# Performance work log

Hardware: AMD Instinct MI355X
Metric: run time of the kernel (lower is better)

## Reference

```python
import jax, jax.numpy as jnp
import numpy as np

M, TS, NX, NY = 24, 60, 192, 192   # solutions, source timesteps, source grid
H, D = 4, 8                         # num_heads, d_head
SIGMA = 0.2
N_TIME_STEPS = 50
T_MAX = 200.0
LX = 100.0                          # solutions[0]['params']['Lx']
SRC_T_MAX = 200.0                   # solutions[0]['params']['t_max']
NG = 50                             # target grid resolution (hard-coded in source)


def setup_inputs():
    key = jax.random.key(0)
    ks = jax.random.split(key, 8)
    c1_preds = jax.random.normal(ks[0], (M, TS, NX, NY), jnp.float32)
    c2_preds = jax.random.normal(ks[1], (M, TS, NX, NY), jnp.float32)
    lys = 30.0 + 90.0 * jax.random.uniform(ks[2], (M,), jnp.float32)
    c_cus = 0.0029 * jax.random.uniform(ks[3], (M,), jnp.float32)
    c_nis = 0.0018 * jax.random.uniform(ks[4], (M,), jnp.float32)
    params = jnp.stack([lys, c_cus, c_nis], axis=1)  # [M,3]
    # nonuniform, sorted per-solution y grid spanning [0, Ly_m]
    base = jnp.linspace(0.0, 1.0, NY, dtype=jnp.float32) ** 1.2
    src_y = lys[:, None] * base[None, :]  # [M,NY]
    src_t_last = 100.0 + 200.0 * jax.random.uniform(ks[5], (M,), jnp.float32)
    Wq = 0.3 * jax.random.normal(ks[6], (3, H * D), jnp.float32)
    Wk = 0.3 * jax.random.normal(ks[7], (3, H * D), jnp.float32)
    bq = jnp.zeros((H * D,), jnp.float32)
    bk = jnp.zeros((H * D,), jnp.float32)
    return dict(c1_preds=c1_preds, c2_preds=c2_preds, params=params, src_y=src_y,
                src_t_last=src_t_last, Wq=Wq, bq=bq, Wk=Wk, bk=bk,
                ly_target=jnp.float32(75.0), c_cu_target=jnp.float32(0.0015),
                c_ni_target=jnp.float32(0.0009))


def _axis_interp(grid, q):
    """1-D linear interp setup. grid [G] sorted, q [P] -> (idx, frac, in_bounds)."""
    G = grid.shape[-1]
    idx = jnp.clip(jnp.searchsorted(grid, q, side='right') - 1, 0, G - 2)
    g0 = jnp.take(grid, idx)
    g1 = jnp.take(grid, idx + 1)
    frac = (q - g0) / (g1 - g0)
    inb = (q >= grid[0]) & (q <= grid[-1])  # scipy fill_value=0 outside
    return idx, frac, inb


def reference(c1_preds, c2_preds, params, src_y, src_t_last, Wq, bq, Wk, bk,
              ly_target, c_cu_target, c_ni_target):
    lys, c_cus, c_nis = params[:, 0], params[:, 1], params[:, 2]
    # normalization exactly as in the torch forward
    ly_n = (lys - 30.0) / (120.0 - 30.0)
    cu_n = c_cus / 0.0029
    ni_n = c_nis / 0.0018
    t_ly = (ly_target - 30.0) / (120.0 - 30.0)
    t_cu = c_cu_target / 0.0029
    t_ni = c_ni_target / 0.0018

    p = jnp.stack([ly_n, cu_n, ni_n], axis=1)            # [M,3]
    tgt = jnp.stack([t_ly, t_cu, t_ni])[None, :]          # [1,3]
    Q = (tgt @ Wq + bq).reshape(H, D)                     # [H,D]
    K = (p @ Wk + bk).reshape(-1, H, D)                   # [M,H,D]
    logits = jnp.einsum('mhd,hd->mh', K, Q) / jnp.sqrt(jnp.float32(D))
    attn = jax.nn.softmax(logits, axis=0).mean(axis=1)    # softmax over solutions, mean heads -> [M]

    dist2 = ((ly_n - t_ly) ** 2 + (cu_n - t_cu) ** 2 + (ni_n - t_ni) ** 2) / SIGMA ** 2
    sw = jnp.exp(-dist2 / 2.0)
    sw = sw / (sw.sum() + 1e-12)
    w = attn * sw
    w = w / (w.sum() + 1e-12)
    w = jax.lax.stop_gradient(w)  # original detaches weights before interpolation

    # ---- physics-aware interpolation ----
    times = jnp.linspace(0.0, min(SRC_T_MAX, T_MAX), N_TIME_STEPS)  # [T]
    ti = jnp.clip(jnp.round(times[:, None] / src_t_last[None, :] * (TS - 1)).astype(jnp.int32),
                  0, TS - 1)                                         # [T,M]

    src_x = jnp.linspace(0.0, LX, NX)
    qx = jnp.linspace(0.0, LX, NG)
    qy = (jnp.arange(NG, dtype=jnp.float32) / (NG - 1)) * ly_target  # linspace(0, ly_target, NG)

    ix, fx, mx = _axis_interp(src_x, qx)                             # [NG] each (shared x grid)
    scale = ly_target / lys                                           # [M]
    y_scaled = src_y * scale[:, None]                                 # [M,NY]
    iy, fy, my = jax.vmap(lambda g: _axis_interp(g, qy))(y_scaled)    # [M,NG] each
    mask = (mx[None, :, None] & my[:, None, :]).astype(c1_preds.dtype)  # [M,NG,NG]

    T = N_TIME_STEPS
    iy_b = jnp.broadcast_to(iy[None, :, None, :], (T, M, NG, NG))
    iy1_b = jnp.broadcast_to((iy + 1)[None, :, None, :], (T, M, NG, NG))

    def interp_field(preds):
        vals = preds[jnp.arange(M)[None, :], ti]                      # [T,M,NX,NY] time gather
        fxc = fx[None, None, :, None]
        vx = vals[:, :, ix, :] * (1.0 - fxc) + vals[:, :, ix + 1, :] * fxc  # [T,M,NG,NY]
        v0 = jnp.take_along_axis(vx, iy_b, axis=3)                    # [T,M,NG,NG]
        v1 = jnp.take_along_axis(vx, iy1_b, axis=3)
        fyc = fy[None, :, None, :]
        v = (v0 * (1.0 - fyc) + v1 * fyc) * mask[None]
        return jnp.einsum('tmij,m->tij', v, w)                        # weighted sum over solutions

    c1 = interp_field(c1_preds).at[:, :, 0].set(c_cu_target)
    c2 = interp_field(c2_preds).at[:, :, -1].set(c_ni_target)
    return jnp.stack([c1, c2])  # [2, T, NG, NG]
```

## Files before the change

kernel.cpp:

```cpp
#include <hip/hip_runtime.h>
#include <math.h>

#define M   24
#define TS  60
#define NX  192
#define NY  192
#define H_  4
#define D_  8
#define NTS 50
#define NG  50

__device__ float g_w[M];
__device__ int   g_ti[NTS][M];
__device__ int   g_ix[NG];
__device__ float g_fx[NG];
__device__ float g_mx[NG];
__device__ int   g_iy[M][NG];
__device__ float g_fy[M][NG];
__device__ float g_my[M][NG];

__global__ __launch_bounds__(256) void prep_init_kernel(
    const float* __restrict__ params, const float* __restrict__ src_y,
    const float* __restrict__ stl,
    const float* __restrict__ Wq, const float* __restrict__ bq,
    const float* __restrict__ Wk, const float* __restrict__ bk,
    const float* __restrict__ lyt_p, const float* __restrict__ ccu_p,
    const float* __restrict__ cni_p,
    float* __restrict__ out)
{
    const int tid = threadIdx.x;

    if (blockIdx.x > 0) {
        const int idx = (blockIdx.x - 1) * blockDim.x + tid;
        const int total = 2 * NTS * NG * NG;
        if (idx < total) {
            const int j = idx % NG;
            const int f = idx / (NTS * NG * NG);
            float v = 0.0f;
            if (f == 0 && j == 0)    v = ccu_p[0];
            if (f == 1 && j == NG-1) v = cni_p[0];
            out[idx] = v;
        }
        return;
    }

    __shared__ float s_logits[M][H_];
    __shared__ float s_sw[M];

    const float ly_target = lyt_p[0];
    const float c_cu_t = ccu_p[0];
    const float c_ni_t = cni_p[0];

    const float t_ly = (ly_target - 30.0f) / 90.0f;
    const float t_cu = c_cu_t / 0.0029f;
    const float t_ni = c_ni_t / 0.0018f;

    if (tid < M) {
        const int m = tid;
        const float ly  = params[m*3 + 0];
        const float ccu = params[m*3 + 1];
        const float cni = params[m*3 + 2];
        const float ly_n = (ly - 30.0f) / 90.0f;
        const float cu_n = ccu / 0.0029f;
        const float ni_n = cni / 0.0018f;
        for (int h = 0; h < H_; ++h) {
            float acc = 0.0f;
            for (int d = 0; d < D_; ++d) {
                const int col = h*D_ + d;
                const float q = t_ly*Wq[0*32+col] + t_cu*Wq[1*32+col] + t_ni*Wq[2*32+col] + bq[col];
                const float k = ly_n*Wk[0*32+col] + cu_n*Wk[1*32+col] + ni_n*Wk[2*32+col] + bk[col];
                acc += k * q;
            }
            s_logits[m][h] = acc / sqrtf(8.0f);
        }
        const float dly = ly_n - t_ly, dcu = cu_n - t_cu, dni = ni_n - t_ni;
        const float d2 = (dly*dly + dcu*dcu + dni*dni) / 0.04f;
        s_sw[m] = expf(-d2 * 0.5f);
    }
    __syncthreads();

    if (tid == 0) {
        float attn[M];
        for (int m = 0; m < M; ++m) attn[m] = 0.0f;
        for (int h = 0; h < H_; ++h) {
            float mxv = -1e30f;
            for (int m = 0; m < M; ++m) mxv = fmaxf(mxv, s_logits[m][h]);
            float e[M]; float s = 0.0f;
            for (int m = 0; m < M; ++m) { e[m] = expf(s_logits[m][h] - mxv); s += e[m]; }
            for (int m = 0; m < M; ++m) attn[m] += e[m] / s;
        }
        float ssw = 0.0f;
        for (int m = 0; m < M; ++m) ssw += s_sw[m];
        float w[M]; float wsum = 0.0f;
        for (int m = 0; m < M; ++m) {
            w[m] = (attn[m] * 0.25f) * (s_sw[m] / (ssw + 1e-12f));
            wsum += w[m];
        }
        for (int m = 0; m < M; ++m) g_w[m] = w[m] / (wsum + 1e-12f);
    }

    const float step_t = 200.0f / 49.0f;
    for (int idx = tid; idx < NTS*M; idx += blockDim.x) {
        const int t = idx / M, m = idx % M;
        const float tt = (t == NTS-1) ? 200.0f : step_t * (float)t;
        const float r = tt / stl[m] * 59.0f;
        int ti = (int)rintf(r);
        ti = ti < 0 ? 0 : (ti > TS-1 ? TS-1 : ti);
        g_ti[t][m] = ti;
    }

    if (tid < NG) {
        const int i = tid;
        const float step_x = 100.0f / 191.0f;
        const float step_q = 100.0f / 49.0f;
        const float q = (i == NG-1) ? 100.0f : step_q * (float)i;
        int pos = 0;
        for (int g = 0; g < NX; ++g) {
            const float gv = (g == NX-1) ? 100.0f : step_x * (float)g;
            if (gv <= q) pos = g + 1;
        }
        int id = pos - 1;
        id = id < 0 ? 0 : (id > NX-2 ? NX-2 : id);
        const float g0 = (id   == NX-1) ? 100.0f : step_x * (float)id;
        const float g1 = (id+1 == NX-1) ? 100.0f : step_x * (float)(id+1);
        g_ix[i] = id;
        g_fx[i] = (q - g0) / (g1 - g0);
        g_mx[i] = (q >= 0.0f && q <= 100.0f) ? 1.0f : 0.0f;
    }

    for (int idx = tid; idx < M*NG; idx += blockDim.x) {
        const int m = idx / NG, j = idx % NG;
        const float scale = ly_target / params[m*3 + 0];
        const float q = (float)j / 49.0f * ly_target;
        const float* sy = src_y + m*NY;
        int pos = 0;
        for (int g = 0; g < NY; ++g) {
            const float gv = sy[g] * scale;
            if (gv <= q) pos = g + 1;
        }
        int id = pos - 1;
        id = id < 0 ? 0 : (id > NY-2 ? NY-2 : id);
        const float g0 = sy[id] * scale;
        const float g1 = sy[id+1] * scale;
        g_iy[m][j] = id;
        g_fy[m][j] = (q - g0) / (g1 - g0);
        const float gfirst = sy[0] * scale;
        const float glast  = sy[NY-1] * scale;
        g_my[m][j] = (q >= gfirst && q <= glast) ? 1.0f : 0.0f;
    }
}

__global__ __launch_bounds__(256) void interp_kernel(
    const float* __restrict__ c1, const float* __restrict__ c2,
    float* __restrict__ out)
{
    const int m = blockIdx.x;
    const int t = blockIdx.y;
    const int f = blockIdx.z;
    const int tid = threadIdx.x;

    __shared__ float xrow[NG][NY + 1];

    const float* __restrict__ preds = (f == 0) ? c1 : c2;
    const int tim = g_ti[t][m];
    const float* __restrict__ slice = preds + (((size_t)m * TS + tim) * NX) * (size_t)NY;

    for (int idx = tid; idx < NG * (NY / 4); idx += blockDim.x) {
        const int i  = idx / (NY / 4);
        const int y4 = (idx - i * (NY / 4)) * 4;
        const int   ixi = g_ix[i];
        const float fxi = g_fx[i];
        const float4 r0 = *(const float4*)(slice + (size_t)ixi * NY + y4);
        const float4 r1 = *(const float4*)(slice + (size_t)(ixi + 1) * NY + y4);
        xrow[i][y4 + 0] = r0.x * (1.0f - fxi) + r1.x * fxi;
        xrow[i][y4 + 1] = r0.y * (1.0f - fxi) + r1.y * fxi;
        xrow[i][y4 + 2] = r0.z * (1.0f - fxi) + r1.z * fxi;
        xrow[i][y4 + 3] = r0.w * (1.0f - fxi) + r1.w * fxi;
    }
    __syncthreads();

    const float wm = g_w[m];
    for (int idx = tid; idx < NG * NG; idx += blockDim.x) {
        const int i = idx / NG;
        const int j = idx - i * NG;
        if ((f == 0 && j == 0) || (f == 1 && j == NG - 1)) continue;
        const int   iyj = g_iy[m][j];
        const float fyj = g_fy[m][j];
        const float msk = g_mx[i] * g_my[m][j];
        const float v0 = xrow[i][iyj];
        const float v1 = xrow[i][iyj + 1];
        const float v = (v0 * (1.0f - fyj) + v1 * fyj) * msk;
        atomicAdd(&out[(((size_t)f * NTS + t) * NG + i) * NG + j], v * wm);
    }
}

extern "C" void kernel_launch(void* const* d_in, const int* in_sizes, int n_in,
                              void* d_out, int out_size, void* d_ws, size_t ws_size,
                              hipStream_t stream) {
    const float* c1     = (const float*)d_in[0];
    const float* c2     = (const float*)d_in[1];
    const float* params = (const float*)d_in[2];
    const float* src_y  = (const float*)d_in[3];
    const float* stl    = (const float*)d_in[4];
    const float* Wq     = (const float*)d_in[5];
    const float* bq     = (const float*)d_in[6];
    const float* Wk     = (const float*)d_in[7];
    const float* bk     = (const float*)d_in[8];
    const float* lyt    = (const float*)d_in[9];
    const float* ccut   = (const float*)d_in[10];
    const float* cnit   = (const float*)d_in[11];
    float* out = (float*)d_out;

    const int total = 2 * NTS * NG * NG;
    const int init_blocks = (total + 255) / 256;
    prep_init_kernel<<<1 + init_blocks, 256, 0, stream>>>(
        params, src_y, stl, Wq, bq, Wk, bk, lyt, ccut, cnit, out);

    dim3 grid(M, NTS, 2);
    interp_kernel<<<grid, 256, 0, stream>>>(c1, c2, out);
}
```

Before: 436.8 us.

## Replace atomic accumulation with per-solution partial buffers and a reduce kernel

Instead of each (m,t,f) block atomically adding weighted values into the output, each block now writes its weighted slab to a workspace partial buffer, and a separate reduce kernel sums over the 24 solutions and applies the boundary overrides. The zero-init pass is dropped from the prep kernel. The shared-memory row is padded to allow float4 stores. This removes atomic contention, at the cost of writing and re-reading a 24x larger intermediate (about 29 MB) and an extra launch.

```diff
diff --git a/kernel.cpp b/kernel.cpp
--- a/kernel.cpp
+++ b/kernel.cpp
@@ -19,31 +19,15 @@
 __device__ float g_fy[M][NG];
 __device__ float g_my[M][NG];
 
-__global__ __launch_bounds__(256) void prep_init_kernel(
+__global__ __launch_bounds__(256) void prep_kernel(
     const float* __restrict__ params, const float* __restrict__ src_y,
     const float* __restrict__ stl,
     const float* __restrict__ Wq, const float* __restrict__ bq,
     const float* __restrict__ Wk, const float* __restrict__ bk,
     const float* __restrict__ lyt_p, const float* __restrict__ ccu_p,
-    const float* __restrict__ cni_p,
-    float* __restrict__ out)
+    const float* __restrict__ cni_p)
 {
     const int tid = threadIdx.x;
-
-    if (blockIdx.x > 0) {
-        const int idx = (blockIdx.x - 1) * blockDim.x + tid;
-        const int total = 2 * NTS * NG * NG;
-        if (idx < total) {
-            const int j = idx % NG;
-            const int f = idx / (NTS * NG * NG);
-            float v = 0.0f;
-            if (f == 0 && j == 0)    v = ccu_p[0];
-            if (f == 1 && j == NG-1) v = cni_p[0];
-            out[idx] = v;
-        }
-        return;
-    }
-
     __shared__ float s_logits[M][H_];
     __shared__ float s_sw[M];
 
@@ -150,48 +134,72 @@
     }
 }
 
-__global__ __launch_bounds__(256) void interp_kernel(
+__global__ __launch_bounds__(256) void stage_kernel(
     const float* __restrict__ c1, const float* __restrict__ c2,
-    float* __restrict__ out)
+    float* __restrict__ partial)
 {
     const int m = blockIdx.x;
     const int t = blockIdx.y;
     const int f = blockIdx.z;
     const int tid = threadIdx.x;
 
-    __shared__ float xrow[NG][NY + 1];
+    __shared__ float xrow[NG][NY + 4];
 
     const float* __restrict__ preds = (f == 0) ? c1 : c2;
     const int tim = g_ti[t][m];
     const float* __restrict__ slice = preds + (((size_t)m * TS + tim) * NX) * (size_t)NY;
 
-    for (int idx = tid; idx < NG * (NY / 4); idx += blockDim.x) {
+    for (int idx = tid; idx < NG * (NY / 4); idx += 256) {
         const int i  = idx / (NY / 4);
         const int y4 = (idx - i * (NY / 4)) * 4;
         const int   ixi = g_ix[i];
         const float fxi = g_fx[i];
         const float4 r0 = *(const float4*)(slice + (size_t)ixi * NY + y4);
         const float4 r1 = *(const float4*)(slice + (size_t)(ixi + 1) * NY + y4);
-        xrow[i][y4 + 0] = r0.x * (1.0f - fxi) + r1.x * fxi;
-        xrow[i][y4 + 1] = r0.y * (1.0f - fxi) + r1.y * fxi;
-        xrow[i][y4 + 2] = r0.z * (1.0f - fxi) + r1.z * fxi;
-        xrow[i][y4 + 3] = r0.w * (1.0f - fxi) + r1.w * fxi;
+        float4 v;
+        v.x = r0.x * (1.0f - fxi) + r1.x * fxi;
+        v.y = r0.y * (1.0f - fxi) + r1.y * fxi;
+        v.z = r0.z * (1.0f - fxi) + r1.z * fxi;
+        v.w = r0.w * (1.0f - fxi) + r1.w * fxi;
+        *(float4*)&xrow[i][y4] = v;
     }
     __syncthreads();
 
     const float wm = g_w[m];
-    for (int idx = tid; idx < NG * NG; idx += blockDim.x) {
+    float* __restrict__ dst = partial + (((size_t)f * NTS + t) * M + m) * (size_t)(NG * NG);
+    for (int idx = tid; idx < NG * NG; idx += 256) {
         const int i = idx / NG;
         const int j = idx - i * NG;
-        if ((f == 0 && j == 0) || (f == 1 && j == NG - 1)) continue;
         const int   iyj = g_iy[m][j];
         const float fyj = g_fy[m][j];
         const float msk = g_mx[i] * g_my[m][j];
         const float v0 = xrow[i][iyj];
         const float v1 = xrow[i][iyj + 1];
         const float v = (v0 * (1.0f - fyj) + v1 * fyj) * msk;
-        atomicAdd(&out[(((size_t)f * NTS + t) * NG + i) * NG + j], v * wm);
-    }
+        dst[idx] = v * wm;
+    }
+}
+
+__global__ __launch_bounds__(256) void reduce_kernel(
+    const float* __restrict__ partial, float* __restrict__ out,
+    const float* __restrict__ ccu_p, const float* __restrict__ cni_p)
+{
+    const int idx = blockIdx.x * 256 + threadIdx.x;
+    const int total = 2 * NTS * NG * NG;
+    if (idx >= total) return;
+    const int p  = idx % (NG * NG);
+    const int ft = idx / (NG * NG);
+    const int f  = ft / NTS;
+    const int j  = p % NG;
+
+    const float* __restrict__ src = partial + (size_t)ft * M * (NG * NG) + p;
+    float acc = 0.0f;
+    #pragma unroll
+    for (int m = 0; m < M; ++m) acc += src[(size_t)m * (NG * NG)];
+
+    if (f == 0 && j == 0)      acc = ccu_p[0];
+    if (f == 1 && j == NG - 1) acc = cni_p[0];
+    out[idx] = acc;
 }
 
 extern "C" void kernel_launch(void* const* d_in, const int* in_sizes, int n_in,
@@ -209,13 +217,14 @@
     const float* lyt    = (const float*)d_in[9];
     const float* ccut   = (const float*)d_in[10];
     const float* cnit   = (const float*)d_in[11];
-    float* out = (float*)d_out;
+    float* out     = (float*)d_out;
+    float* partial = (float*)d_ws;
+
+    prep_kernel<<<1, 256, 0, stream>>>(params, src_y, stl, Wq, bq, Wk, bk, lyt, ccut, cnit);
+
+    dim3 gridA(M, NTS, 2);
+    stage_kernel<<<gridA, 256, 0, stream>>>(c1, c2, partial);
 
     const int total = 2 * NTS * NG * NG;
-    const int init_blocks = (total + 255) / 256;
-    prep_init_kernel<<<1 + init_blocks, 256, 0, stream>>>(
-        params, src_y, stl, Wq, bq, Wk, bk, lyt, ccut, cnit, out);
-
-    dim3 grid(M, NTS, 2);
-    interp_kernel<<<grid, 256, 0, stream>>>(c1, c2, out);
-}
+    reduce_kernel<<<(total + 255) / 256, 256, 0, stream>>>(partial, out, ccut, cnit);
+}
```

Measured after the change: 432.0 us. About the same (-1.1%).
